# Kernel optimization log

Measured on AMD Instinct MI355X. Metric: run time of the kernel, lower is better.

## Reference

```python
import jax, jax.numpy as jnp
import numpy as np

# ---- Clifford algebra Cl(4,1) setup -------------------------------------
SIG = [1, 1, 1, 1, -1]
GA = 1 << len(SIG)  # 32
B, S, E, H = 2, 512, 256, 8
HD = E // H


def _cayley_sign(sig):
    """sign[a,b] such that e_a * e_b = sign[a,b] * e_(a XOR b)."""
    n = len(sig)
    G = 1 << n
    M = np.zeros((G, G), np.float32)
    for a in range(G):
        for b in range(G):
            # canonical reordering sign
            ss = 0
            aa = a >> 1
            while aa:
                ss += bin(aa & b).count('1')
                aa >>= 1
            s = -1.0 if (ss & 1) else 1.0
            # metric contraction on shared basis vectors
            common = a & b
            for i in range(n):
                if (common >> i) & 1:
                    s *= sig[i]
            M[a, b] = s
    return M

SIGN = _cayley_sign(SIG)          # [GA, GA]
SIG_DIAG = np.diag(SIGN).copy()   # blade square signs (metric diagonal)


def _manifold_norm(x):
    # normalize each multivector over its GA components
    return x / jnp.sqrt(jnp.sum(x * x, axis=-1, keepdims=True) + 1e-6)


def _geo_linear(x, w):
    """Clifford linear layer: out[...,o,l] = sum_{i,m,n: m^n=l} w[o,i,m] x[...,i,n] sign(m,n).
    x: [B,S,In,GA], w: [Out,In,GA]. Loop over 32 fixed blades (signed permutation + GEMM)."""
    G = x.shape[-1]
    out = 0.0
    for m in range(G):
        perm = np.arange(G) ^ m              # n = m ^ l
        coeff = jnp.asarray(SIGN[m, perm])   # sign(m, n)
        xs = x[..., perm] * coeff            # [B,S,In,GA]
        out = out + jnp.einsum('oi,bsil->bsol', w[:, :, m], xs)
    return out


def _versor_linear(x, w):
    return _manifold_norm(_geo_linear(x, w))


def _forward(x, mask, wq, wk, wv, wo, gamma):
    b, s = x.shape[0], x.shape[1]
    q = _versor_linear(x, wq).reshape(b, s, H, HD, GA).transpose(0, 2, 1, 3, 4)
    k = _versor_linear(x, wk).reshape(b, s, H, HD, GA).transpose(0, 2, 1, 3, 4)
    v = _versor_linear(x, wv).reshape(b, s, H, HD, GA).transpose(0, 2, 1, 3, 4)
    q_flat = q.reshape(b * H, s, HD, GA)
    k_flat = k.reshape(b * H, s, HD, GA)
    sig_diag = jnp.asarray(SIG_DIAG)
    q_sig = q_flat * sig_diag                      # metric-weighted query
    scalar_score = jnp.einsum('bidl,bjdl->bij', q_sig, k_flat)   # [BH,S,S]
    q_norm_sq = jnp.sum(q_flat ** 2, axis=(-1, -2))[:, :, None]  # [BH,S,1]
    k_norm_sq = jnp.sum(k_flat ** 2, axis=(-1, -2))[:, None, :]  # [BH,1,S]
    bivector_norm = jnp.sqrt(jax.nn.relu(q_norm_sq * k_norm_sq - scalar_score ** 2) + 1e-6)
    score = (scalar_score + gamma * bivector_norm) / np.float32(np.sqrt(HD))
    # triangle update (seq > 1)
    score = score + 0.1 * jnp.matmul(jax.nn.softmax(score, axis=-1), score)
    score = score.reshape(b, H, s, s)
    score = jnp.where(mask[:, None, None, :] == 0, jnp.float32(-1e9), score)
    attn_probs = jax.nn.softmax(score, axis=-1)
    out = jnp.einsum('bhij,bhjdl->bhidl', attn_probs, v)
    out = out.transpose(0, 2, 1, 3, 4).reshape(b, s, E, GA)
    return _versor_linear(out, wo)


def setup_inputs() -> dict:
    key = jax.random.key(0)
    ks = jax.random.split(key, 6)
    std = np.float32((2.0 / (E * GA)) ** 0.5)
    x = jax.random.normal(ks[0], (B, S, E, GA), dtype=jnp.float32)
    wq = jax.random.normal(ks[1], (E, E, GA), dtype=jnp.float32) * std
    wk = jax.random.normal(ks[2], (E, E, GA), dtype=jnp.float32) * std
    wv = jax.random.normal(ks[3], (E, E, GA), dtype=jnp.float32) * std
    wo = jax.random.normal(ks[4], (E, E, GA), dtype=jnp.float32) * std
    gamma = jnp.asarray(0.1, dtype=jnp.float32)
    mask = jnp.ones((B, S), dtype=jnp.int32)
    return {'x': x, 'wq': wq, 'wk': wk, 'wv': wv, 'wo': wo, 'gamma': gamma, 'mask': mask}


def reference(x, wq, wk, wv, wo, gamma, mask):
    return _forward(x, mask, wq, wk, wv, wo, gamma)
```

## Files before the change

kernel.cpp:

```cpp
#include <hip/hip_runtime.h>
#include <stdint.h>

typedef unsigned short u16;
typedef unsigned int u32;
typedef __attribute__((ext_vector_type(8))) __bf16 bf16x8;
typedef __attribute__((ext_vector_type(4))) float f32x4;

#define DEVINL __device__ __forceinline__

DEVINL float bf2f(u16 u){ union{u32 i; float f;} c; c.i = ((u32)u)<<16; return c.f; }
DEVINL u16 f2bf(float f){ union{float f; u32 i;} c; c.f=f; u32 u=c.i; return (u16)((u + 0x7fffu + ((u>>16)&1u))>>16); }
DEVINL u32 pack2(float a, float b){ return (u32)f2bf(a) | ((u32)f2bf(b)<<16); }

DEVINL int sign_neg(int a, int b){
  int s = __popc((a>>1)&b) + __popc((a>>2)&b) + __popc((a>>3)&b) + __popc((a>>4)&b) + ((a&b)>>4);
  return s & 1;
}

struct GTab { int col[32][4]; int ph[32][4]; };
constexpr GTab make_gtab(){
  GTab g{};
  int gc[5][4] = {}; int gp[5][4] = {};
  for (int r=0;r<4;r++){
    const int a=(r>>1)&1, b=r&1;
    gc[0][r]=r^2; gp[0][r]=0;
    gc[1][r]=r^2; gp[1][r]= a?1:3;
    gc[2][r]=r^1; gp[2][r]= a?2:0;
    gc[3][r]=r^1; gp[3][r]=((a?2:0)+(b?1:3))&3;
    gc[4][r]=r;   gp[4][r]=(3+(a?2:0)+(b?2:0))&3;
  }
  for (int I=0;I<32;I++){
    for (int r=0;r<4;r++){ g.col[I][r]=r; g.ph[I][r]=0; }
    for (int bit=0;bit<5;bit++) if ((I>>bit)&1){
      for (int r=0;r<4;r++){
        const int c = g.col[I][r];
        g.ph[I][r]  = (g.ph[I][r] + gp[bit][c]) & 3;
        g.col[I][r] = gc[bit][c];
      }
    }
  }
  return g;
}
constexpr GTab GT = make_gtab();

DEVINL void mv2mat(const float (&x)[32], float (&Mre)[4][4], float (&Mim)[4][4]){
  #pragma unroll
  for (int r=0;r<4;r++)
    #pragma unroll
    for (int c=0;c<4;c++){ Mre[r][c]=0.f; Mim[r][c]=0.f; }
  #pragma unroll
  for (int l=0;l<32;l++){
    #pragma unroll
    for (int r=0;r<4;r++){
      constexpr const GTab& G = GT;
      const int c = G.col[l][r], p = G.ph[l][r];
      if (p==0) Mre[r][c] += x[l];
      else if (p==1) Mim[r][c] += x[l];
      else if (p==2) Mre[r][c] -= x[l];
      else Mim[r][c] -= x[l];
    }
  }
}

DEVINL void mat2mv(const float (&v)[4][8], float (&x)[32]){
  #pragma unroll
  for (int l=0;l<32;l++){
    float s = 0.f;
    #pragma unroll
    for (int r=0;r<4;r++){
      constexpr const GTab& G = GT;
      const int c = G.col[l][r], p = G.ph[l][r];
      if (p==0) s += v[c][r];
      else if (p==1) s += v[c][4+r];
      else if (p==2) s -= v[c][r];
      else s -= v[c][4+r];
    }
    x[l] = 0.25f*s;
  }
}

DEVINL void gload_lds16(const void* g, void* l){
  __builtin_amdgcn_global_load_lds(
    (const __attribute__((address_space(1))) void*)g,
    (__attribute__((address_space(3))) void*)l, 16, 0, 0);
}

__global__ __launch_bounds__(256) void k_v2m(const float* __restrict__ x, u16* __restrict__ Am){
  const int bs = blockIdx.x, i = threadIdx.x;
  const float* xp = x + ((size_t)bs*256 + i)*32;
  float xv[32];
  #pragma unroll
  for (int q=0;q<8;q++){
    float4 v = *(const float4*)(xp + q*4);
    xv[q*4+0]=v.x; xv[q*4+1]=v.y; xv[q*4+2]=v.z; xv[q*4+3]=v.w;
  }
  float Mre[4][4], Mim[4][4];
  mv2mat(xv, Mre, Mim);
  #pragma unroll
  for (int c=0;c<4;c++){
    u32 w0 = pack2(Mre[0][c], Mre[1][c]);
    u32 w1 = pack2(Mre[2][c], Mre[3][c]);
    u32 w2 = pack2(Mim[0][c], Mim[1][c]);
    u32 w3 = pack2(Mim[2][c], Mim[3][c]);
    *(uint4*)(Am + ((size_t)(bs*4+c))*2048 + i*8) = make_uint4(w0,w1,w2,w3);
  }
}

__global__ __launch_bounds__(256) void k_w2m(const float* __restrict__ wq, const float* __restrict__ wk,
                                             const float* __restrict__ wv, const float* __restrict__ wo,
                                             u16* __restrict__ Bfo){
  const int bid = blockIdx.x, i = threadIdx.x;
  const int wsel = bid>>8, o = bid&255;
  const float* w = wsel==0?wq: wsel==1?wk: wsel==2?wv: wo;
  const float* wp = w + ((size_t)o*256 + i)*32;
  float wv32[32];
  #pragma unroll
  for (int q=0;q<8;q++){
    float4 v = *(const float4*)(wp + q*4);
    wv32[q*4+0]=v.x; wv32[q*4+1]=v.y; wv32[q*4+2]=v.z; wv32[q*4+3]=v.w;
  }
  float Wre[4][4], Wim[4][4];
  mv2mat(wv32, Wre, Wim);
  u16* base = Bfo + (size_t)wsel*4194304 + (size_t)(i>>3)*131072 + (o>>1)*1024
            + ((i>>2)&1)*512;
  const int lanebase = (o&1)*8 + (i&3)*16;
  #pragma unroll
  for (int r8=0;r8<8;r8++){
    float e0,e1,e2,e3,e4,e5,e6,e7;
    if (r8<4){
      e0=Wre[r8][0]; e1=Wre[r8][1]; e2=Wre[r8][2]; e3=Wre[r8][3];
      e4=-Wim[r8][0]; e5=-Wim[r8][1]; e6=-Wim[r8][2]; e7=-Wim[r8][3];
    } else {
      e0=Wim[r8-4][0]; e1=Wim[r8-4][1]; e2=Wim[r8-4][2]; e3=Wim[r8-4][3];
      e4=Wre[r8-4][0]; e5=Wre[r8-4][1]; e6=Wre[r8-4][2]; e7=Wre[r8-4][3];
    }
    *(uint4*)(base + (lanebase + r8)*8) =
      make_uint4(pack2(e0,e1), pack2(e2,e3), pack2(e4,e5), pack2(e6,e7));
  }
}

DEVINL void mg_phase(int kq, int cbuf, const u16* __restrict__ Wsel, const int (&boff)[4][2],
                     const u16* __restrict__ Am, int row0, int sbase, int lane,
                     u16* SM, uint4 (&B0)[4], uint4 (&B0n)[4],
                     f32x4 (&acc)[4][4], int wm, int wn, int lo, int hi){
  const u16* Wq = Wsel + (size_t)kq*131072;
  uint4 B1[4];
  #pragma unroll
  for (int fn=0; fn<4; ++fn) B1[fn] = *(const uint4*)(Wq + boff[fn][1]);
  asm volatile("s_waitcnt vmcnt(8)" ::: "memory");
  __builtin_amdgcn_sched_barrier(0);
  __builtin_amdgcn_s_barrier();
  __builtin_amdgcn_sched_barrier(0);
  if (kq+1 < 32){
    #pragma unroll
    for (int cc=0;cc<4;cc++){
      const int base = sbase + cc*64;
      const int idx = base + lane;
      const int rr = idx>>3, g = idx&7;
      gload_lds16(Am + (size_t)(row0+rr)*2048 + (kq+1)*64 + ((g^(rr&7))*8),
                  SM + (cbuf^1)*8192 + base*8);
    }
  }
  const u16* Ab = SM + cbuf*8192;
  bf16x8 af0[4];
  #pragma unroll
  for (int f=0;f<4;f++){
    const int ra = wm*64 + f*16 + lo;
    af0[f] = *(const bf16x8*)(Ab + ra*64 + ((hi ^ (ra&7))*8));
  }
  if (kq+1 < 32){
    const u16* Wn = Wq + 131072;
    #pragma unroll
    for (int fn=0; fn<4; ++fn) B0n[fn] = *(const uint4*)(Wn + boff[fn][0]);
  }
  __builtin_amdgcn_s_setprio(1);
  #pragma unroll
  for (int fm=0;fm<4;fm++){
    #pragma unroll
    for (int fn=0;fn<4;fn++)
      acc[fm][fn] = __builtin_amdgcn_mfma_f32_16x16x32_bf16(
          af0[fm], *(const bf16x8*)&B0[fn], acc[fm][fn], 0,0,0);
  }
  __builtin_amdgcn_s_setprio(0);
  bf16x8 af1[4];
  #pragma unroll
  for (int f=0;f<4;f++){
    const int ra = wm*64 + f*16 + lo;
    af1[f] = *(const bf16x8*)(Ab + ra*64 + (((4+hi) ^ (ra&7))*8));
  }
  __builtin_amdgcn_s_setprio(1);
  #pragma unroll
  for (int fm=0;fm<4;fm++){
    #pragma unroll
    for (int fn=0;fn<4;fn++)
      acc[fm][fn] = __builtin_amdgcn_mfma_f32_16x16x32_bf16(
          af1[fm], *(const bf16x8*)&B1[fn], acc[fm][fn], 0,0,0);
  }
  __builtin_amdgcn_s_setprio(0);
}

template<int EPI>
__global__ __launch_bounds__(256) void k_mgemm(const u16* __restrict__ Am, const u16* __restrict__ Bfo,
                                               u16* __restrict__ qkv, float* __restrict__ dout,
                                               float* __restrict__ Nqp, float* __restrict__ Nkp){
  constexpr int NT = (EPI==0)?48:16;
  constexpr int NWG = 32*NT;
  __shared__ __align__(16) u16 SM[128*136];
  const int wg = blockIdx.x;
  const int bid = (wg&7)*(NWG/8) + (wg>>3);
  const int tn = bid>>5, tm = bid&31;
  const int row0 = tm*128, col0 = tn*128;
  const int sel   = (EPI==0)? (col0>>11) : 3;
  const int ncol0 = (EPI==0)? (col0&2047) : col0;
  const u16* Wsel = Bfo + (size_t)sel*4194304;
  const int t = threadIdx.x, lane = t&63, wid = t>>6;
  const int wm = wid>>1, wn = wid&1, lo = lane&15, hi = lane>>4;

  int boff[4][2];
  #pragma unroll
  for (int fn=0; fn<4; ++fn){
    const int nblk = (ncol0>>4) + wn*4 + fn;
    #pragma unroll
    for (int kk=0; kk<2; ++kk)
      boff[fn][kk] = (nblk*2+kk)*512 + lane*8;
  }

  f32x4 acc[4][4];
  #pragma unroll
  for(int a=0;a<4;a++){
    #pragma unroll
    for(int b=0;b<4;b++){ acc[a][b] = (f32x4){0.f,0.f,0.f,0.f}; }
  }

  const int sbase = (wid*4)*64;
  #pragma unroll
  for (int cc=0;cc<4;cc++){
    const int base = sbase + cc*64;
    const int idx = base + lane;
    const int rr = idx>>3, g = idx&7;
    gload_lds16(Am + (size_t)(row0+rr)*2048 + ((g^(rr&7))*8), SM + base*8);
  }
  uint4 B0a[4], B0b[4];
  #pragma unroll
  for (int fn=0; fn<4; ++fn) B0a[fn] = *(const uint4*)(Wsel + boff[fn][0]);

  #pragma unroll 1
  for (int kq2=0; kq2<16; ++kq2){
    mg_phase(2*kq2,   0, Wsel, boff, Am, row0, sbase, lane, SM, B0a, B0b, acc, wm, wn, lo, hi);
    mg_phase(2*kq2+1, 1, Wsel, boff, Am, row0, sbase, lane, SM, B0b, B0a, acc, wm, wn, lo, hi);
  }

  __syncthreads();
  #pragma unroll
  for (int fm=0;fm<4;fm++){
    #pragma unroll
    for (int r=0;r<4;r++){
      const int mL = wm*64 + fm*16 + hi*4 + r;
      #pragma unroll
      for (int fn=0;fn<4;fn++){
        const int nL = wn*64 + fn*16 + lo;
        SM[mL*136 + nL] = f2bf(acc[fm][fn][r]);
      }
    }
  }
  __syncthreads();
  const int bsL = t>>3, oLp = t&7;
  const int bs = (row0>>2) + bsL;
  const int o0w = ncol0>>3;
  float nsum = 0.f;
  #pragma unroll
  for (int u=0;u<2;u++){
    const int oL = oLp + u*8;
    float v[4][8];
    #pragma unroll
    for (int c=0;c<4;c++){
      uint4 q4 = *(const uint4*)(SM + (bsL*4+c)*136 + oL*8);
      v[c][0]=bf2f((u16)(q4.x&0xffffu)); v[c][1]=bf2f((u16)(q4.x>>16));
      v[c][2]=bf2f((u16)(q4.y&0xffffu)); v[c][3]=bf2f((u16)(q4.y>>16));
      v[c][4]=bf2f((u16)(q4.z&0xffffu)); v[c][5]=bf2f((u16)(q4.z>>16));
      v[c][6]=bf2f((u16)(q4.w&0xffffu)); v[c][7]=bf2f((u16)(q4.w>>16));
    }
    float xs[32];
    mat2mv(v, xs);
    float s = 0.f;
    #pragma unroll
    for (int l=0;l<32;l++) s += xs[l]*xs[l];
    const float rs = rsqrtf(s + 1e-6f);
    if constexpr (EPI==0){
      nsum += s/(s+1e-6f);
      if (sel == 0){
        #pragma unroll
        for (int l=0;l<32;l++) xs[l] = sign_neg(l,l)? -xs[l]*rs : xs[l]*rs;
      } else {
        #pragma unroll
        for (int l=0;l<32;l++) xs[l] *= rs;
      }
      u16* dst = qkv + ((size_t)bs*768 + sel*256 + o0w + oL)*32;
      #pragma unroll
      for (int q=0;q<4;q++)
        *(uint4*)(dst + q*8) = make_uint4(pack2(xs[q*8+0],xs[q*8+1]), pack2(xs[q*8+2],xs[q*8+3]),
                                          pack2(xs[q*8+4],xs[q*8+5]), pack2(xs[q*8+6],xs[q*8+7]));
    } else {
      float* dst = dout + ((size_t)bs*256 + o0w + oL)*32;
      #pragma unroll
      for (int q=0;q<8;q++)
        *(float4*)(dst + q*4) = make_float4(xs[q*4+0]*rs, xs[q*4+1]*rs, xs[q*4+2]*rs, xs[q*4+3]*rs);
    }
  }
  if constexpr (EPI==0){
    if (sel < 2){
      nsum += __shfl_xor(nsum,1); nsum += __shfl_xor(nsum,2); nsum += __shfl_xor(nsum,4);
      if ((t&7)==0){
        const int half = (o0w>>4)&1, h = o0w>>5;
        const int b = bs>>9, s_ = bs&511;
        float* nd = (sel==0)? Nqp : Nkp;
        nd[half*8192 + (b*8+h)*512 + s_] = nsum;
      }
    }
  }
}

DEVINL void mm_steps_p(const u16* Abase, int Astride, const u16* Bbase, int Bstride, int ksteps,
                       u16* SM, f32x4 (&acc)[4][4], int lane, int wid){
  const int wm = wid>>1, wn = wid&1, lo = lane&15, hi = lane>>4;
  #pragma unroll
  for (int c=0;c<4;c++){
    const int gb = (wid*4+c)*64;
    const int idx = gb + lane;
    const int r = idx>>3, j = idx&7;
    const int sw = ((j^(r&7))*8);
    gload_lds16(Abase + (size_t)r*Astride + sw, SM + gb*8);
    gload_lds16(Bbase + (size_t)r*Bstride + sw, SM + 16384 + gb*8);
  }
  int cbuf = 0;
  for (int s=0; s<ksteps; ++s){
    asm volatile("s_waitcnt vmcnt(0)" ::: "memory");
    __builtin_amdgcn_sched_barrier(0);
    __builtin_amdgcn_s_barrier();
    __builtin_amdgcn_sched_barrier(0);
    if (s+1 < ksteps){
      const int k0 = (s+1)*64;
      #pragma unroll
      for (int c=0;c<4;c++){
        const int gb = (wid*4+c)*64;
        const int idx = gb + lane;
        const int r = idx>>3, j = idx&7;
        const int sw = ((j^(r&7))*8);
        gload_lds16(Abase + (size_t)r*Astride + k0 + sw, SM + (cbuf^1)*8192 + gb*8);
        gload_lds16(Bbase + (size_t)r*Bstride + k0 + sw, SM + 16384 + (cbuf^1)*8192 + gb*8);
      }
    }
    const u16* Al = SM + cbuf*8192;
    const u16* Blc = SM + 16384 + cbuf*8192;
    #pragma unroll
    for (int kk=0; kk<2; ++kk){
      bf16x8 af[4], bfr[4];
      #pragma unroll
      for (int f=0;f<4;f++){
        const int ra = wm*64 + f*16 + lo;
        const int jc = kk*4 + hi;
        af[f] = *(const bf16x8*)(Al + ra*64 + ((jc^(ra&7))*8));
        const int rb = wn*64 + f*16 + lo;
        bfr[f] = *(const bf16x8*)(Blc + rb*64 + ((jc^(rb&7))*8));
      }
      __builtin_amdgcn_s_setprio(1);
      #pragma unroll
      for (int fm=0;fm<4;fm++){
        #pragma unroll
        for (int fn=0;fn<4;fn++)
          acc[fm][fn] = __builtin_amdgcn_mfma_f32_16x16x32_bf16(af[fm], bfr[fn], acc[fm][fn], 0,0,0);
      }
      __builtin_amdgcn_s_setprio(0);
    }
    cbuf ^= 1;
  }
}

__global__ __launch_bounds__(256) void k_score(const u16* __restrict__ qkv, const float* __restrict__ Nqp,
                                               const float* __restrict__ Nkp, const float* __restrict__ gptr,
                                               float* __restrict__ S1, u16* __restrict__ S1T){
  __shared__ __align__(16) u16 SM[32768];
  u16* Tl = SM;
  const int wg = blockIdx.x;
  const int bid = (wg&7)*32 + (wg>>3);
  const int bh = bid>>4, ti=(bid>>2)&3, tj=bid&3;
  const int b = bh>>3, h = bh&7;
  const int i0=ti*128, j0=tj*128;
  const int t=threadIdx.x, lane=t&63, wid=t>>6;
  const int wm=wid>>1, wn=wid&1, lo=lane&15, hi=lane>>4;
  f32x4 acc[4][4];
  #pragma unroll
  for(int a=0;a<4;a++){
    #pragma unroll
    for(int c=0;c<4;c++){ acc[a][c] = (f32x4){0.f,0.f,0.f,0.f}; }
  }
  const u16* Abase = qkv + ((size_t)(b*512+i0))*24576 + h*1024;
  const u16* Bbase = qkv + ((size_t)(b*512+j0))*24576 + 8192 + h*1024;
  mm_steps_p(Abase, 24576, Bbase, 24576, 16, SM, acc, lane, wid);
  __syncthreads();
  const float gamma = *gptr;
  const float rhd = 0.17677669529663687f;
  float nkv[4];
  #pragma unroll
  for (int fn=0;fn<4;fn++){
    const int idx = bh*512 + j0 + wn*64 + fn*16 + lo;
    nkv[fn] = Nkp[idx] + Nkp[8192 + idx];
  }
  #pragma unroll
  for (int fm=0;fm<4;fm++){
    #pragma unroll
    for (int r=0;r<4;r++){
      const int iL = wm*64 + fm*16 + hi*4 + r;
      const int qidx = bh*512 + i0 + iL;
      const float nq = Nqp[qidx] + Nqp[8192 + qidx];
      #pragma unroll
      for (int fn=0;fn<4;fn++){
        const int jL = wn*64 + fn*16 + lo;
        const float ss = acc[fm][fn][r];
        const float biv = sqrtf(fmaxf(nq*nkv[fn] - ss*ss, 0.f) + 1e-6f);
        const float sc = (ss + gamma*biv)*rhd;
        S1[((size_t)bh*512 + i0 + iL)*512 + j0 + jL] = sc;
        Tl[jL*136 + iL] = f2bf(sc);
      }
    }
  }
  __syncthreads();
  const int jj = t>>1, half = t&1;
  u16* dst = S1T + ((size_t)bh*512 + (j0+jj))*512 + i0 + half*64;
  #pragma unroll
  for (int q=0;q<8;q++)
    *(uint4*)(dst + q*8) = *(const uint4*)(Tl + jj*136 + half*64 + q*8);
}

__global__ __launch_bounds__(256) void k_softmax(const float* __restrict__ S, const int* __restrict__ mask,
                                                 u16* __restrict__ P, int masked){
  const int t = threadIdx.x, lane = t&63, wid = t>>6;
  const int row = blockIdx.x*4 + wid;
  const int b = row>>12;
  const float* sp = S + (size_t)row*512;
  float4 a = *(const float4*)(sp + lane*4);
  float4 c = *(const float4*)(sp + 256 + lane*4);
  if (masked){
    const int* mp = mask + b*512;
    int4 ma = *(const int4*)(mp + lane*4);
    int4 mc = *(const int4*)(mp + 256 + lane*4);
    if (ma.x==0) a.x=-1e9f; if (ma.y==0) a.y=-1e9f; if (ma.z==0) a.z=-1e9f; if (ma.w==0) a.w=-1e9f;
    if (mc.x==0) c.x=-1e9f; if (mc.y==0) c.y=-1e9f; if (mc.z==0) c.z=-1e9f; if (mc.w==0) c.w=-1e9f;
  }
  float mx = fmaxf(fmaxf(fmaxf(a.x,a.y),fmaxf(a.z,a.w)), fmaxf(fmaxf(c.x,c.y),fmaxf(c.z,c.w)));
  #pragma unroll
  for (int o=1;o<64;o<<=1) mx = fmaxf(mx, __shfl_xor(mx,o));
  const float e0=__expf(a.x-mx), e1=__expf(a.y-mx), e2=__expf(a.z-mx), e3=__expf(a.w-mx);
  const float e4=__expf(c.x-mx), e5=__expf(c.y-mx), e6=__expf(c.z-mx), e7=__expf(c.w-mx);
  float sm = (e0+e1)+(e2+e3)+(e4+e5)+(e6+e7);
  #pragma unroll
  for (int o=1;o<64;o<<=1) sm += __shfl_xor(sm,o);
  const float inv = 1.f/sm;
  u16* pp = P + (size_t)row*512;
  *(uint2*)(pp + lane*4)       = make_uint2(pack2(e0*inv,e1*inv), pack2(e2*inv,e3*inv));
  *(uint2*)(pp + 256 + lane*4) = make_uint2(pack2(e4*inv,e5*inv), pack2(e6*inv,e7*inv));
}

__global__ __launch_bounds__(256) void k_tri(const u16* __restrict__ P1, const u16* __restrict__ S1T,
                                             float* __restrict__ S1){
  __shared__ __align__(16) u16 SM[32768];
  const int wg = blockIdx.x;
  const int bid = (wg&7)*32 + (wg>>3);
  const int bh = bid>>4, ti=(bid>>2)&3, tj=bid&3;
  const int i0=ti*128, j0=tj*128;
  const int t=threadIdx.x, lane=t&63, wid=t>>6;
  const int wm=wid>>1, wn=wid&1, lo=lane&15, hi=lane>>4;
  f32x4 acc[4][4];
  #pragma unroll
  for(int a=0;a<4;a++){
    #pragma unroll
    for(int c=0;c<4;c++){ acc[a][c] = (f32x4){0.f,0.f,0.f,0.f}; }
  }
  const u16* Abase = P1  + ((size_t)bh*512 + i0)*512;
  const u16* Bbase = S1T + ((size_t)bh*512 + j0)*512;
  mm_steps_p(Abase, 512, Bbase, 512, 8, SM, acc, lane, wid);
  #pragma unroll
  for (int fm=0;fm<4;fm++){
    #pragma unroll
    for (int r=0;r<4;r++){
      const int iL = wm*64 + fm*16 + hi*4 + r;
      #pragma unroll
      for (int fn=0;fn<4;fn++){
        const int jL = wn*64 + fn*16 + lo;
        const size_t idx = ((size_t)bh*512 + i0 + iL)*512 + j0 + jL;
        S1[idx] = S1[idx] + 0.1f*acc[fm][fn][r];
      }
    }
  }
}

__global__ __launch_bounds__(256) void k_tr_v(const u16* __restrict__ qkv, u16* __restrict__ VT){
  __shared__ u16 tile[128*129];
  const int bid=blockIdx.x;
  const int bh = bid>>5, dch=(bid>>2)&7, sch=bid&3;
  const int b=bh>>3, h=bh&7;
  const int d0=dch*128, s0=sch*128;
  const int t=threadIdx.x;
  {
    const int r=t>>1, half=t&1;
    const u16* src = qkv + ((size_t)(b*512+s0+r))*24576 + 16384 + h*1024 + d0 + half*64;
    #pragma unroll
    for (int q=0;q<8;q++){
      uint4 v = *(const uint4*)(src + q*8);
      u16* dp = tile + r*129 + half*64 + q*8;
      dp[0]=(u16)(v.x&0xffffu); dp[1]=(u16)(v.x>>16); dp[2]=(u16)(v.y&0xffffu); dp[3]=(u16)(v.y>>16);
      dp[4]=(u16)(v.z&0xffffu); dp[5]=(u16)(v.z>>16); dp[6]=(u16)(v.w&0xffffu); dp[7]=(u16)(v.w>>16);
    }
  }
  __syncthreads();
  {
    const int rr=t>>1, half=t&1;
    u16* dst = VT + ((size_t)bh*1024 + d0+rr)*512 + s0 + half*64;
    #pragma unroll
    for (int q=0;q<4;q++){
      u32 w[8];
      #pragma unroll
      for (int e=0;e<8;e++){
        const int s = half*64 + q*16 + e*2;
        w[e] = (u32)tile[s*129+rr] | ((u32)tile[(s+1)*129+rr]<<16);
      }
      *(uint4*)(dst + q*16)     = make_uint4(w[0],w[1],w[2],w[3]);
      *(uint4*)(dst + q*16 + 8) = make_uint4(w[4],w[5],w[6],w[7]);
    }
  }
}

__global__ __launch_bounds__(256) void k_pv(const u16* __restrict__ P2, const u16* __restrict__ VT,
                                            u16* __restrict__ Am2){
  __shared__ __align__(16) u16 SM[32768];
  u16* Tl = SM;
  const int wg = blockIdx.x;
  const int bid = (wg&7)*64 + (wg>>3);
  const int bh = bid>>5, ti=(bid>>3)&3, td=bid&7;
  const int b=bh>>3, h=bh&7;
  const int i0=ti*128, d0=td*128;
  const int t=threadIdx.x, lane=t&63, wid=t>>6;
  const int wm=wid>>1, wn=wid&1, lo=lane&15, hi=lane>>4;
  f32x4 acc[4][4];
  #pragma unroll
  for(int a=0;a<4;a++){
    #pragma unroll
    for(int c=0;c<4;c++){ acc[a][c] = (f32x4){0.f,0.f,0.f,0.f}; }
  }
  const u16* Abase = P2 + ((size_t)bh*512 + i0)*512;
  const u16* Bbase = VT + ((size_t)bh*1024 + d0)*512;
  mm_steps_p(Abase, 512, Bbase, 512, 8, SM, acc, lane, wid);
  __syncthreads();
  #pragma unroll
  for (int fm=0;fm<4;fm++){
    #pragma unroll
    for (int r=0;r<4;r++){
      const int sL = wm*64 + fm*16 + hi*4 + r;
      #pragma unroll
      for (int fn=0;fn<4;fn++){
        const int dL = wn*64 + fn*16 + lo;
        Tl[sL*136 + dL] = f2bf(acc[fm][fn][r]);
      }
    }
  }
  __syncthreads();
  #pragma unroll
  for (int u=0;u<2;u++){
    const int idx = t + u*256;
    const int sL = idx>>2, hdL = idx&3;
    const u16* tp = Tl + sL*136 + hdL*32;
    float xv[32];
    #pragma unroll
    for (int q=0;q<4;q++){
      uint4 v = *(const uint4*)(tp + q*8);
      xv[q*8+0]=bf2f((u16)(v.x&0xffffu)); xv[q*8+1]=bf2f((u16)(v.x>>16));
      xv[q*8+2]=bf2f((u16)(v.y&0xffffu)); xv[q*8+3]=bf2f((u16)(v.y>>16));
      xv[q*8+4]=bf2f((u16)(v.z&0xffffu)); xv[q*8+5]=bf2f((u16)(v.z>>16));
      xv[q*8+6]=bf2f((u16)(v.w&0xffffu)); xv[q*8+7]=bf2f((u16)(v.w>>16));
    }
    float Mre[4][4], Mim[4][4];
    mv2mat(xv, Mre, Mim);
    const int e = h*32 + td*4 + hdL;
    const size_t mrow = ((size_t)(b*512 + i0 + sL))*4;
    #pragma unroll
    for (int c=0;c<4;c++){
      u32 w0 = pack2(Mre[0][c], Mre[1][c]);
      u32 w1 = pack2(Mre[2][c], Mre[3][c]);
      u32 w2 = pack2(Mim[0][c], Mim[1][c]);
      u32 w3 = pack2(Mim[2][c], Mim[3][c]);
      *(uint4*)(Am2 + (mrow + c)*2048 + e*8) = make_uint4(w0,w1,w2,w3);
    }
  }
}

extern "C" void kernel_launch(void* const* d_in, const int* in_sizes, int n_in,
                              void* d_out, int out_size, void* d_ws, size_t ws_size,
                              hipStream_t stream) {
  const float* x  = (const float*)d_in[0];
  const float* wq = (const float*)d_in[1];
  const float* wk = (const float*)d_in[2];
  const float* wv = (const float*)d_in[3];
  const float* wo = (const float*)d_in[4];
  const float* gamma = (const float*)d_in[5];
  const int*   mask  = (const int*)d_in[6];
  float* out = (float*)d_out;

  char* ws = (char*)d_ws;
  size_t off = 0;
  auto alloc = [&](size_t n){ char* p = ws + off; off += (n + 255) & ~(size_t)255; return p; };
  u16*  Am  = (u16*) alloc(16777216);
  u16*  Bfo = (u16*) alloc(33554432);
  u16*  qkv = (u16*) alloc(50331648);
  float* Nqp = (float*)alloc(65536);
  float* Nkp = (float*)alloc(65536);
  float* S1 = (float*)alloc(16777216);
  u16*  S1T = (u16*) alloc(8388608);
  u16*  P2  = (u16*) alloc(8388608);
  u16*  P1  = (u16*)Am;
  u16*  VT  = (u16*)S1;
  u16*  Am2 = (u16*)Am;

  k_v2m<<<1024, 256, 0, stream>>>(x, Am);
  k_w2m<<<1024, 256, 0, stream>>>(wq, wk, wv, wo, Bfo);
  k_mgemm<0><<<1536, 256, 0, stream>>>(Am, Bfo, qkv, nullptr, Nqp, Nkp);
  k_score<<<256, 256, 0, stream>>>(qkv, Nqp, Nkp, gamma, S1, S1T);
  k_softmax<<<2048, 256, 0, stream>>>(S1, mask, P1, 0);
  k_tri<<<256, 256, 0, stream>>>(P1, S1T, S1);
  k_softmax<<<2048, 256, 0, stream>>>(S1, mask, P2, 1);
  k_tr_v<<<512, 256, 0, stream>>>(qkv, VT);
  k_pv<<<512, 256, 0, stream>>>(P2, VT, Am2);
  k_mgemm<1><<<512, 256, 0, stream>>>(Am2, Bfo, nullptr, out, nullptr, nullptr);
}
```

Baseline: 264.0 us.

## Stage GEMM B tiles through LDS with double-buffered async loads

The B-operand weight fragments were loaded straight from global memory into registers with software prefetching. They are now staged into a double-buffered LDS region with the same async global-to-LDS path used for A, and each wave reads its fragments from LDS. Each wave's B reads are redundant across the two wm waves, so sharing through LDS cuts global traffic. In exchange the kernel uses more LDS (64 KB), which may reduce occupancy, and it now waits on vmcnt(0) every k-step, giving up the finer overlap of the earlier pipeline.

```diff
diff --git a/kernel.cpp b/kernel.cpp
--- a/kernel.cpp
+++ b/kernel.cpp
@@ -139,91 +139,22 @@
   }
 }
 
-DEVINL void mg_phase(int kq, int cbuf, const u16* __restrict__ Wsel, const int (&boff)[4][2],
-                     const u16* __restrict__ Am, int row0, int sbase, int lane,
-                     u16* SM, uint4 (&B0)[4], uint4 (&B0n)[4],
-                     f32x4 (&acc)[4][4], int wm, int wn, int lo, int hi){
-  const u16* Wq = Wsel + (size_t)kq*131072;
-  uint4 B1[4];
-  #pragma unroll
-  for (int fn=0; fn<4; ++fn) B1[fn] = *(const uint4*)(Wq + boff[fn][1]);
-  asm volatile("s_waitcnt vmcnt(8)" ::: "memory");
-  __builtin_amdgcn_sched_barrier(0);
-  __builtin_amdgcn_s_barrier();
-  __builtin_amdgcn_sched_barrier(0);
-  if (kq+1 < 32){
-    #pragma unroll
-    for (int cc=0;cc<4;cc++){
-      const int base = sbase + cc*64;
-      const int idx = base + lane;
-      const int rr = idx>>3, g = idx&7;
-      gload_lds16(Am + (size_t)(row0+rr)*2048 + (kq+1)*64 + ((g^(rr&7))*8),
-                  SM + (cbuf^1)*8192 + base*8);
-    }
-  }
-  const u16* Ab = SM + cbuf*8192;
-  bf16x8 af0[4];
-  #pragma unroll
-  for (int f=0;f<4;f++){
-    const int ra = wm*64 + f*16 + lo;
-    af0[f] = *(const bf16x8*)(Ab + ra*64 + ((hi ^ (ra&7))*8));
-  }
-  if (kq+1 < 32){
-    const u16* Wn = Wq + 131072;
-    #pragma unroll
-    for (int fn=0; fn<4; ++fn) B0n[fn] = *(const uint4*)(Wn + boff[fn][0]);
-  }
-  __builtin_amdgcn_s_setprio(1);
-  #pragma unroll
-  for (int fm=0;fm<4;fm++){
-    #pragma unroll
-    for (int fn=0;fn<4;fn++)
-      acc[fm][fn] = __builtin_amdgcn_mfma_f32_16x16x32_bf16(
-          af0[fm], *(const bf16x8*)&B0[fn], acc[fm][fn], 0,0,0);
-  }
-  __builtin_amdgcn_s_setprio(0);
-  bf16x8 af1[4];
-  #pragma unroll
-  for (int f=0;f<4;f++){
-    const int ra = wm*64 + f*16 + lo;
-    af1[f] = *(const bf16x8*)(Ab + ra*64 + (((4+hi) ^ (ra&7))*8));
-  }
-  __builtin_amdgcn_s_setprio(1);
-  #pragma unroll
-  for (int fm=0;fm<4;fm++){
-    #pragma unroll
-    for (int fn=0;fn<4;fn++)
-      acc[fm][fn] = __builtin_amdgcn_mfma_f32_16x16x32_bf16(
-          af1[fm], *(const bf16x8*)&B1[fn], acc[fm][fn], 0,0,0);
-  }
-  __builtin_amdgcn_s_setprio(0);
-}
-
 template<int EPI>
 __global__ __launch_bounds__(256) void k_mgemm(const u16* __restrict__ Am, const u16* __restrict__ Bfo,
                                                u16* __restrict__ qkv, float* __restrict__ dout,
                                                float* __restrict__ Nqp, float* __restrict__ Nkp){
   constexpr int NT = (EPI==0)?48:16;
   constexpr int NWG = 32*NT;
-  __shared__ __align__(16) u16 SM[128*136];
+  __shared__ __align__(16) u16 SM[32768];
   const int wg = blockIdx.x;
   const int bid = (wg&7)*(NWG/8) + (wg>>3);
   const int tn = bid>>5, tm = bid&31;
   const int row0 = tm*128, col0 = tn*128;
   const int sel   = (EPI==0)? (col0>>11) : 3;
   const int ncol0 = (EPI==0)? (col0&2047) : col0;
-  const u16* Wsel = Bfo + (size_t)sel*4194304;
+  const u16* Wsel = Bfo + (size_t)sel*4194304 + (size_t)(ncol0>>4)*1024;
   const int t = threadIdx.x, lane = t&63, wid = t>>6;
   const int wm = wid>>1, wn = wid&1, lo = lane&15, hi = lane>>4;
-
-  int boff[4][2];
-  #pragma unroll
-  for (int fn=0; fn<4; ++fn){
-    const int nblk = (ncol0>>4) + wn*4 + fn;
-    #pragma unroll
-    for (int kk=0; kk<2; ++kk)
-      boff[fn][kk] = (nblk*2+kk)*512 + lane*8;
-  }
 
   f32x4 acc[4][4];
   #pragma unroll
@@ -239,15 +170,52 @@
     const int idx = base + lane;
     const int rr = idx>>3, g = idx&7;
     gload_lds16(Am + (size_t)(row0+rr)*2048 + ((g^(rr&7))*8), SM + base*8);
-  }
-  uint4 B0a[4], B0b[4];
-  #pragma unroll
-  for (int fn=0; fn<4; ++fn) B0a[fn] = *(const uint4*)(Wsel + boff[fn][0]);
-
-  #pragma unroll 1
-  for (int kq2=0; kq2<16; ++kq2){
-    mg_phase(2*kq2,   0, Wsel, boff, Am, row0, sbase, lane, SM, B0a, B0b, acc, wm, wn, lo, hi);
-    mg_phase(2*kq2+1, 1, Wsel, boff, Am, row0, sbase, lane, SM, B0b, B0a, acc, wm, wn, lo, hi);
+    const int bidx = cc*256 + t;
+    gload_lds16(Wsel + bidx*8, SM + 16384 + bidx*8);
+  }
+
+  int cbuf = 0;
+  for (int kq=0; kq<32; ++kq){
+    asm volatile("s_waitcnt vmcnt(0)" ::: "memory");
+    __builtin_amdgcn_sched_barrier(0);
+    __builtin_amdgcn_s_barrier();
+    __builtin_amdgcn_sched_barrier(0);
+    if (kq+1 < 32){
+      const u16* WqB = Wsel + (size_t)(kq+1)*131072;
+      #pragma unroll
+      for (int cc=0;cc<4;cc++){
+        const int base = sbase + cc*64;
+        const int idx = base + lane;
+        const int rr = idx>>3, g = idx&7;
+        gload_lds16(Am + (size_t)(row0+rr)*2048 + (kq+1)*64 + ((g^(rr&7))*8),
+                    SM + (cbuf^1)*8192 + base*8);
+        const int bidx = cc*256 + t;
+        gload_lds16(WqB + bidx*8, SM + 16384 + (cbuf^1)*8192 + bidx*8);
+      }
+    }
+    const u16* Ab = SM + cbuf*8192;
+    const u16* Blc = SM + 16384 + cbuf*8192;
+    #pragma unroll
+    for (int kk=0; kk<2; ++kk){
+      bf16x8 af[4], bfr[4];
+      #pragma unroll
+      for (int f=0;f<4;f++){
+        const int ra = wm*64 + f*16 + lo;
+        const int jc = kk*4 + hi;
+        af[f] = *(const bf16x8*)(Ab + ra*64 + ((jc^(ra&7))*8));
+        bfr[f] = *(const bf16x8*)(Blc + ((wn*4+f)*2+kk)*512 + lane*8);
+      }
+      __builtin_amdgcn_s_setprio(1);
+      #pragma unroll
+      for (int fm=0;fm<4;fm++){
+        #pragma unroll
+        for (int fn=0;fn<4;fn++)
+          acc[fm][fn] = __builtin_amdgcn_mfma_f32_16x16x32_bf16(
+              af[fm], bfr[fn], acc[fm][fn], 0,0,0);
+      }
+      __builtin_amdgcn_s_setprio(0);
+    }
+    cbuf ^= 1;
   }
 
   __syncthreads();
```

After: 265.4 us. No clear change (+0.5%).
